# Kernel tuning notes

Measured on AMD Instinct MI355X. Metric: run time of the kernel, lower is better.

## Reference

```python
import jax, jax.numpy as jnp
import numpy as np

TAKE = 64
HID = 64


def setup_inputs() -> dict:
    key = jax.random.key(0)
    ks = jax.random.split(key, 12)
    B, N, C = 32, 1000, 1601
    s = 1.0 / np.sqrt(C)
    s2 = 1.0 / np.sqrt(HID)
    return {
        "class_logits": jax.random.normal(ks[0], (B, N, C), dtype=jnp.float32),
        "proposals": jax.random.uniform(ks[1], (B, N, 4), dtype=jnp.float32),
        # subject projection (Linear stored as [in, out] so y = x @ W + b)
        "Ws1": jax.random.uniform(ks[2], (C, HID), minval=-s, maxval=s),
        "bs1": jax.random.uniform(ks[3], (HID,), minval=-s, maxval=s),
        "Ws2": jax.random.uniform(ks[4], (HID, HID), minval=-s2, maxval=s2),
        "bs2": jax.random.uniform(ks[5], (HID,), minval=-s2, maxval=s2),
        # object projection
        "Wo1": jax.random.uniform(ks[6], (C, HID), minval=-s, maxval=s),
        "bo1": jax.random.uniform(ks[7], (HID,), minval=-s, maxval=s),
        "Wo2": jax.random.uniform(ks[8], (HID, HID), minval=-s2, maxval=s2),
        "bo2": jax.random.uniform(ks[9], (HID,), minval=-s2, maxval=s2),
    }


def _mlp(x, W1, b1, W2, b2):
    # Linear -> ReLU -> Linear
    return jnp.maximum(x @ W1 + b1, 0.0) @ W2 + b2


def reference(class_logits, proposals, Ws1, bs1, Ws2, bs2, Wo1, bo1, Wo2, bo2):
    B, N, _ = class_logits.shape
    subj = _mlp(class_logits, Ws1, bs1, Ws2, bs2)  # [B, N, 64]
    obj = _mlp(class_logits, Wo1, bo1, Wo2, bo2)   # [B, N, 64]
    # relatedness[b, i, j] = sigmoid(<subj_i, obj_j>)
    scores = jax.nn.sigmoid(jnp.einsum("bnd,bmd->bnm", subj, obj))  # [B, N, N]
    flat = scores.reshape(B, N * N)
    top_scores, top_idx = jax.lax.top_k(flat, TAKE)  # descending, same as sort[:take]
    # flat index k = subject*N + object (row-major), matching the torch meshgrid
    pairs = jnp.stack([top_idx // N, top_idx % N], axis=-1)  # [B, 64, 2] (subj, obj)
    return pairs, top_scores
```

## Files before the change

kernel.cpp:

```cpp
#include <hip/hip_runtime.h>
#include <cstdint>

#define NB 32
#define NN 1000
#define NC 1601
#define HID 64
#define ROWS (NB*NN)
#define CAPB 15360
#define SROWS 15
#define NBIN 4096
#define KCH 32
#define RB 64
#define TPB 256
#define XSTR 68
#define WSTR 132
#define SSTR 132

__device__ __forceinline__ uint32_t f2key(float f){
  uint32_t u = __float_as_uint(f);
  return (u & 0x80000000u) ? ~u : (u | 0x80000000u);
}
__device__ __forceinline__ float key2f(uint32_t k){
  uint32_t u = (k & 0x80000000u) ? (k & 0x7fffffffu) : ~k;
  return __uint_as_float(u);
}

__global__ __launch_bounds__(TPB, 2) void mlp_kernel(
    const float* __restrict__ x,
    const float* __restrict__ Ws1, const float* __restrict__ bs1,
    const float* __restrict__ Ws2, const float* __restrict__ bs2,
    const float* __restrict__ Wo1, const float* __restrict__ bo1,
    const float* __restrict__ Wo2, const float* __restrict__ bo2,
    float* __restrict__ subj, float* __restrict__ obj)
{
  __shared__ float smem[2*KCH*XSTR + 2*KCH*WSTR];
  __shared__ float xtail[RB];
  const int tid = threadIdx.x;
  const int tx  = tid & 15;
  const int ty  = tid >> 4;
  const int row0 = blockIdx.x * RB;

  float* xbuf = smem;
  float* wbuf = smem + 2*KCH*XSTR;

  float accS[4][4], accO[4][4];
  #pragma unroll
  for (int r=0;r<4;r++)
    #pragma unroll
    for (int c=0;c<4;c++){ accS[r][c]=0.f; accO[r][c]=0.f; }

  float  xstg[8];
  float4 wstg[4];
  #pragma unroll
  for (int it=0; it<8; it++){
    int u = tid + it*TPB;
    xstg[it] = x[(size_t)(row0 + (u>>5))*NC + (u&31)];
  }
  #pragma unroll
  for (int it=0; it<4; it++){
    int u = tid + it*TPB;
    int k = u>>5, c4 = u&31;
    const float* src = (c4 < 16) ? (Ws1 + (size_t)k*HID + c4*4)
                                 : (Wo1 + (size_t)k*HID + (c4-16)*4);
    wstg[it] = *(const float4*)src;
  }

  const int NCHUNK = 50;
  for (int c = 0; c < NCHUNK; c++){
    float* xT = xbuf + (c & 1)*(KCH*XSTR);
    float* wC = wbuf + (c & 1)*(KCH*WSTR);
    #pragma unroll
    for (int it=0; it<8; it++){
      int u = tid + it*TPB;
      xT[(u&31)*XSTR + (u>>5)] = xstg[it];
    }
    #pragma unroll
    for (int it=0; it<4; it++){
      int u = tid + it*TPB;
      *(float4*)&wC[(u>>5)*WSTR + (u&31)*4] = wstg[it];
    }
    __syncthreads();
    if (c+1 < NCHUNK){
      const int k0n = (c+1)*KCH;
      #pragma unroll
      for (int it=0; it<8; it++){
        int u = tid + it*TPB;
        xstg[it] = x[(size_t)(row0 + (u>>5))*NC + k0n + (u&31)];
      }
      #pragma unroll
      for (int it=0; it<4; it++){
        int u = tid + it*TPB;
        int k = u>>5, c4 = u&31;
        const float* src = (c4 < 16) ? (Ws1 + (size_t)(k0n+k)*HID + c4*4)
                                     : (Wo1 + (size_t)(k0n+k)*HID + (c4-16)*4);
        wstg[it] = *(const float4*)src;
      }
    }
    #pragma unroll 4
    for (int k=0; k<KCH; k++){
      float4 a  = *(const float4*)&xT[k*XSTR + ty*4];
      float4 bS = *(const float4*)&wC[k*WSTR + tx*4];
      float4 bO = *(const float4*)&wC[k*WSTR + 64 + tx*4];
      float av[4] = {a.x,a.y,a.z,a.w};
      float bs_[4] = {bS.x,bS.y,bS.z,bS.w};
      float bo_[4] = {bO.x,bO.y,bO.z,bO.w};
      #pragma unroll
      for (int r=0;r<4;r++)
        #pragma unroll
        for (int c2=0;c2<4;c2++){
          accS[r][c2] = fmaf(av[r], bs_[c2], accS[r][c2]);
          accO[r][c2] = fmaf(av[r], bo_[c2], accO[r][c2]);
        }
    }
  }

  if (tid < RB) xtail[tid] = x[(size_t)(row0 + tid)*NC + 1600];
  __syncthreads();
  {
    float4 a  = *(const float4*)&xtail[ty*4];
    float4 bS = *(const float4*)(Ws1 + (size_t)1600*HID + tx*4);
    float4 bO = *(const float4*)(Wo1 + (size_t)1600*HID + tx*4);
    float av[4] = {a.x,a.y,a.z,a.w};
    float bs_[4] = {bS.x,bS.y,bS.z,bS.w};
    float bo_[4] = {bO.x,bO.y,bO.z,bO.w};
    #pragma unroll
    for (int r=0;r<4;r++)
      #pragma unroll
      for (int c2=0;c2<4;c2++){
        accS[r][c2] = fmaf(av[r], bs_[c2], accS[r][c2]);
        accO[r][c2] = fmaf(av[r], bo_[c2], accO[r][c2]);
      }
  }

  float* hTS = smem;
  float* hTO = smem + 64*XSTR;
  __syncthreads();
  #pragma unroll
  for (int jj=0; jj<4; jj++){
    float bS = bs1[tx*4 + jj];
    float bO = bo1[tx*4 + jj];
    float4 hv;
    hv.x = fmaxf(accS[0][jj]+bS, 0.f); hv.y = fmaxf(accS[1][jj]+bS, 0.f);
    hv.z = fmaxf(accS[2][jj]+bS, 0.f); hv.w = fmaxf(accS[3][jj]+bS, 0.f);
    *(float4*)&hTS[(tx*4+jj)*XSTR + ty*4] = hv;
    hv.x = fmaxf(accO[0][jj]+bO, 0.f); hv.y = fmaxf(accO[1][jj]+bO, 0.f);
    hv.z = fmaxf(accO[2][jj]+bO, 0.f); hv.w = fmaxf(accO[3][jj]+bO, 0.f);
    *(float4*)&hTO[(tx*4+jj)*XSTR + ty*4] = hv;
  }
  __syncthreads();

  float accYS[4][4], accYO[4][4];
  #pragma unroll
  for (int c2=0;c2<4;c2++){
    float bvS = bs2[tx*4 + c2];
    float bvO = bo2[tx*4 + c2];
    #pragma unroll
    for (int r=0;r<4;r++){ accYS[r][c2] = bvS; accYO[r][c2] = bvO; }
  }
  #pragma unroll 4
  for (int d=0; d<64; d++){
    float4 aS = *(const float4*)&hTS[d*XSTR + ty*4];
    float4 aO = *(const float4*)&hTO[d*XSTR + ty*4];
    float4 wS = *(const float4*)(Ws2 + (size_t)d*HID + tx*4);
    float4 wO = *(const float4*)(Wo2 + (size_t)d*HID + tx*4);
    float aSv[4] = {aS.x,aS.y,aS.z,aS.w};
    float aOv[4] = {aO.x,aO.y,aO.z,aO.w};
    float wSv[4] = {wS.x,wS.y,wS.z,wS.w};
    float wOv[4] = {wO.x,wO.y,wO.z,wO.w};
    #pragma unroll
    for (int r=0;r<4;r++)
      #pragma unroll
      for (int c2=0;c2<4;c2++){
        accYS[r][c2] = fmaf(aSv[r], wSv[c2], accYS[r][c2]);
        accYO[r][c2] = fmaf(aOv[r], wOv[c2], accYO[r][c2]);
      }
  }
  #pragma unroll
  for (int r=0;r<4;r++){
    *(float4*)&subj[(size_t)(row0 + ty*4 + r)*HID + tx*4] =
      make_float4(accYS[r][0], accYS[r][1], accYS[r][2], accYS[r][3]);
    *(float4*)&obj[(size_t)(row0 + ty*4 + r)*HID + tx*4] =
      make_float4(accYO[r][0], accYO[r][1], accYO[r][2], accYO[r][3]);
  }
}

__global__ __launch_bounds__(1024, 4) void sample_thresh(
    const float* __restrict__ subj, const float* __restrict__ obj,
    uint32_t* __restrict__ L)
{
  __shared__ float sRows[SROWS*HID];
  __shared__ uint32_t keys[SROWS*NN];
  __shared__ uint32_t hist[256];
  __shared__ uint32_t sb[2];
  const int b = blockIdx.x, tid = threadIdx.x;

  const float4* sp = (const float4*)(subj + (size_t)b*NN*HID);
  if (tid < SROWS*16) ((float4*)sRows)[tid] = sp[tid];
  __syncthreads();

  for (int j = tid; j < NN; j += 1024){
    const float4* op4 = (const float4*)(obj + ((size_t)b*NN + j)*HID);
    float4 o[16];
    #pragma unroll
    for (int q=0;q<16;q++) o[q] = op4[q];
    #pragma unroll 1
    for (int i=0;i<SROWS;i++){
      const float4* s4 = (const float4*)(sRows + i*HID);
      float acc = 0.f;
      #pragma unroll
      for (int q=0;q<16;q++){
        float4 s = s4[q];
        acc = fmaf(s.x, o[q].x, acc); acc = fmaf(s.y, o[q].y, acc);
        acc = fmaf(s.z, o[q].z, acc); acc = fmaf(s.w, o[q].w, acc);
      }
      keys[i*NN + j] = f2key(acc);
    }
  }
  __syncthreads();

  uint32_t prefix = 0; int remaining = 64;
  for (int round = 0; round < 2; round++){
    const int shift = 24 - round*8;
    if (tid < 256) hist[tid] = 0;
    __syncthreads();
    for (int idx = tid; idx < SROWS*NN; idx += 1024){
      uint32_t k = keys[idx];
      bool match = (round == 0) || ((k >> 24) == (prefix >> 24));
      if (match) atomicAdd(&hist[(k >> shift) & 255u], 1u);
    }
    __syncthreads();
    if (tid == 0){
      uint32_t cum = 0; int bin = 255;
      for (;; bin--){ cum += hist[bin]; if (cum >= (uint32_t)remaining || bin == 0) break; }
      sb[0] = (uint32_t)bin;
      sb[1] = (uint32_t)(remaining - (int)(cum - hist[bin]));
    }
    __syncthreads();
    prefix |= sb[0] << shift;
    remaining = (int)sb[1];
    __syncthreads();
  }
  if (tid == 0) L[b] = prefix;
}

__device__ __forceinline__ void score_tile_acc(
    const float* __restrict__ subj, const float* __restrict__ obj,
    int b, int ti, int tj, int tid,
    float* __restrict__ sT, float* __restrict__ oT, float (&acc)[8][8])
{
  const int tx = tid & 15, ty = tid >> 4;
  #pragma unroll
  for (int a=0;a<8;a++)
    #pragma unroll
    for (int c=0;c<8;c++) acc[a][c] = 0.f;

  #pragma unroll 1
  for (int half = 0; half < 2; half++){
    __syncthreads();
    {
      const float4* gp = (const float4*)subj;
      #pragma unroll
      for (int it=0; it<4; it++){
        int u = tid + it*256;
        int r = u >> 3, q = (u & 7) + half*8;
        int gr = b*NN + ti + r; gr = gr < ROWS ? gr : (ROWS-1);
        float4 v = gp[(size_t)gr*16 + q];
        int kk = (u & 7)*4;
        sT[(kk+0)*SSTR + r] = v.x;
        sT[(kk+1)*SSTR + r] = v.y;
        sT[(kk+2)*SSTR + r] = v.z;
        sT[(kk+3)*SSTR + r] = v.w;
      }
      const float4* gp2 = (const float4*)obj;
      #pragma unroll
      for (int it=0; it<4; it++){
        int u = tid + it*256;
        int r = u >> 3, q = (u & 7) + half*8;
        int gr = b*NN + tj + r; gr = gr < ROWS ? gr : (ROWS-1);
        float4 v = gp2[(size_t)gr*16 + q];
        int kk = (u & 7)*4;
        oT[(kk+0)*SSTR + r] = v.x;
        oT[(kk+1)*SSTR + r] = v.y;
        oT[(kk+2)*SSTR + r] = v.z;
        oT[(kk+3)*SSTR + r] = v.w;
      }
    }
    __syncthreads();
    #pragma unroll 2
    for (int k=0; k<32; k++){
      float4 s0 = *(const float4*)&sT[k*SSTR + ty*8];
      float4 s1 = *(const float4*)&sT[k*SSTR + ty*8 + 4];
      float4 o0 = *(const float4*)&oT[k*SSTR + tx*8];
      float4 o1 = *(const float4*)&oT[k*SSTR + tx*8 + 4];
      float s[8] = {s0.x,s0.y,s0.z,s0.w,s1.x,s1.y,s1.z,s1.w};
      float o[8] = {o0.x,o0.y,o0.z,o0.w,o1.x,o1.y,o1.z,o1.w};
      #pragma unroll
      for (int a=0;a<8;a++)
        #pragma unroll
        for (int c=0;c<8;c++)
          acc[a][c] = fmaf(s[a], o[c], acc[a][c]);
    }
  }
}

__global__ __launch_bounds__(256, 3) void score_pass1(
    const float* __restrict__ subj, const float* __restrict__ obj,
    const uint32_t* __restrict__ L, uint32_t* __restrict__ cnt,
    uint2* __restrict__ cand, uint32_t* __restrict__ ghist)
{
  __shared__ float sT[32*SSTR];
  __shared__ float oT[32*SSTR];
  __shared__ uint32_t hist[NBIN];
  __shared__ uint32_t lcnt, gbase;
  const int blk = blockIdx.x;
  const int b   = blk >> 6;
  const int t   = blk & 63;
  const int ti  = (t >> 3) << 7;
  const int tj  = (t & 7)  << 7;
  const int tid = threadIdx.x;
  const int tx = tid & 15, ty = tid >> 4;

  for (int i = tid; i < NBIN; i += 256) hist[i] = 0;
  if (tid == 0) lcnt = 0;

  float acc[8][8];
  score_tile_acc(subj, obj, b, ti, tj, tid, sT, oT, acc);

  const uint32_t Lb = L[b];
  int myCnt = 0;
  #pragma unroll
  for (int a=0;a<8;a++){
    int gi = ti + ty*8 + a;
    #pragma unroll
    for (int c=0;c<8;c++){
      int gj = tj + tx*8 + c;
      if (gi < NN && gj < NN){
        uint32_t key = f2key(acc[a][c]);
        if (key >= Lb){ myCnt++; atomicAdd(&hist[key >> 20], 1u); }
      }
    }
  }
  uint32_t lbase = atomicAdd(&lcnt, (uint32_t)myCnt);
  __syncthreads();
  if (tid == 0) gbase = atomicAdd(&cnt[b], lcnt);
  __syncthreads();
  uint32_t pos = gbase + lbase;
  #pragma unroll
  for (int a=0;a<8;a++){
    int gi = ti + ty*8 + a;
    #pragma unroll
    for (int c=0;c<8;c++){
      int gj = tj + tx*8 + c;
      if (gi < NN && gj < NN){
        uint32_t key = f2key(acc[a][c]);
        if (key >= Lb){
          if (pos < CAPB) cand[(size_t)b*CAPB + pos] = make_uint2(key, (uint32_t)(gi*NN + gj));
          pos++;
        }
      }
    }
  }
  __syncthreads();
  for (int i = tid; i < NBIN; i += 256){
    uint32_t v = hist[i];
    if (v) atomicAdd(&ghist[(size_t)b*NBIN + i], v);
  }
}

__global__ __launch_bounds__(256, 1) void pick_thresh(
    const uint32_t* __restrict__ ghist, const uint32_t* __restrict__ cnt,
    uint32_t* __restrict__ T, uint32_t* __restrict__ flag)
{
  __shared__ uint32_t S[256];
  const int b = blockIdx.x, tid = threadIdx.x;
  const uint32_t* h = ghist + (size_t)b*NBIN;
  uint32_t loc[16];
  uint32_t s = 0;
  #pragma unroll
  for (int i=0;i<16;i++){ loc[i] = h[tid*16 + i]; s += loc[i]; }
  S[tid] = s;
  __syncthreads();
  for (int off = 1; off < 256; off <<= 1){
    uint32_t v = (tid + off < 256) ? S[tid + off] : 0u;
    __syncthreads();
    S[tid] += v;
    __syncthreads();
  }
  uint32_t above = (tid < 255) ? S[tid + 1] : 0u;
  if (above < 64u && S[tid] >= 64u){
    uint32_t suf = above; int best = 0;
    for (int i=15;i>=0;i--){ suf += loc[i]; if (suf >= 64u){ best = i; break; } }
    T[b] = (uint32_t)(tid*16 + best) << 20;
  }
  if (tid == 0) flag[b] = (cnt[b] > (uint32_t)CAPB) ? 1u : 0u;
}

__global__ __launch_bounds__(256, 3) void score_repair(
    const float* __restrict__ subj, const float* __restrict__ obj,
    const uint32_t* __restrict__ T, const uint32_t* __restrict__ flag,
    uint32_t* __restrict__ cnt2, uint2* __restrict__ cand)
{
  const int blk = blockIdx.x;
  const int b   = blk >> 6;
  if (flag[b] == 0u) return;

  __shared__ float sT[32*SSTR];
  __shared__ float oT[32*SSTR];
  __shared__ uint32_t lcnt, gbase;
  const int t   = blk & 63;
  const int ti  = (t >> 3) << 7;
  const int tj  = (t & 7)  << 7;
  const int tid = threadIdx.x;
  const int tx = tid & 15, ty = tid >> 4;

  if (tid == 0) lcnt = 0;

  float acc[8][8];
  score_tile_acc(subj, obj, b, ti, tj, tid, sT, oT, acc);

  const uint32_t Tb = T[b];
  int myCnt = 0;
  #pragma unroll
  for (int a=0;a<8;a++){
    int gi = ti + ty*8 + a;
    #pragma unroll
    for (int c=0;c<8;c++){
      int gj = tj + tx*8 + c;
      if (gi < NN && gj < NN && f2key(acc[a][c]) >= Tb) myCnt++;
    }
  }
  uint32_t lbase = atomicAdd(&lcnt, (uint32_t)myCnt);
  __syncthreads();
  if (tid == 0) gbase = atomicAdd(&cnt2[b], lcnt);
  __syncthreads();
  uint32_t pos = gbase + lbase;
  #pragma unroll
  for (int a=0;a<8;a++){
    int gi = ti + ty*8 + a;
    #pragma unroll
    for (int c=0;c<8;c++){
      int gj = tj + tx*8 + c;
      if (gi < NN && gj < NN){
        uint32_t key = f2key(acc[a][c]);
        if (key >= Tb){
          if (pos < CAPB) cand[(size_t)b*CAPB + pos] = make_uint2(key, (uint32_t)(gi*NN + gj));
          pos++;
        }
      }
    }
  }
}

__global__ __launch_bounds__(1024, 4) void final_select(
    const uint32_t* __restrict__ cnt, const uint32_t* __restrict__ cnt2,
    const uint32_t* __restrict__ flag, const uint2* __restrict__ cand,
    float* __restrict__ out)
{
  __shared__ uint32_t keys[CAPB];
  __shared__ uint32_t hist[256];
  __shared__ uint32_t sb[2];
  __shared__ uint2 win[192];
  __shared__ uint32_t wn;
  const int b = blockIdx.x, tid = threadIdx.x;
  uint32_t n0 = flag[b] ? cnt2[b] : cnt[b];
  const int n = (n0 < (uint32_t)CAPB) ? (int)n0 : CAPB;

  for (int i = tid; i < n; i += 1024) keys[i] = cand[(size_t)b*CAPB + i].x;
  if (tid == 0) wn = 0;
  __syncthreads();

  uint32_t prefix = 0; int remaining = 64;
  for (int round = 0; round < 4; round++){
    const int shift = 24 - round*8;
    if (tid < 256) hist[tid] = 0;
    __syncthreads();
    for (int i = tid; i < n; i += 1024){
      uint32_t k = keys[i];
      bool match = (round == 0) || ((k >> (shift+8)) == (prefix >> (shift+8)));
      if (match) atomicAdd(&hist[(k >> shift) & 255u], 1u);
    }
    __syncthreads();
    if (tid == 0){
      uint32_t cum = 0; int bin = 255;
      for (;; bin--){ cum += hist[bin]; if (cum >= (uint32_t)remaining || bin == 0) break; }
      sb[0] = (uint32_t)bin;
      sb[1] = (uint32_t)(remaining - (int)(cum - hist[bin]));
    }
    __syncthreads();
    prefix |= sb[0] << shift;
    remaining = (int)sb[1];
    __syncthreads();
  }
  const uint32_t Tk = prefix;

  for (int i = tid; i < n; i += 1024){
    if (keys[i] >= Tk){
      uint32_t p = atomicAdd(&wn, 1u);
      if (p < 192u) win[p] = make_uint2(keys[i], cand[(size_t)b*CAPB + i].y);
    }
  }
  __syncthreads();
  const int m = (wn < 192u) ? (int)wn : 192;

  if (tid < m){
    const uint64_t me = ((uint64_t)win[tid].x << 32) | (uint64_t)(uint32_t)(~win[tid].y);
    int rank = 0;
    for (int s = 0; s < m; s++){
      uint64_t oth = ((uint64_t)win[s].x << 32) | (uint64_t)(uint32_t)(~win[s].y);
      rank += (oth > me) ? 1 : 0;
    }
    if (rank < 64){
      const uint32_t f = win[tid].y;
      const float d  = key2f(win[tid].x);
      const float sc = 1.0f / (1.0f + expf(-d));
      out[((size_t)b*64 + rank)*2 + 0] = (float)(f / NN);
      out[((size_t)b*64 + rank)*2 + 1] = (float)(f % NN);
      out[(size_t)NB*64*2 + (size_t)b*64 + rank] = sc;
    }
  }
}

extern "C" void kernel_launch(void* const* d_in, const int* in_sizes, int n_in,
                              void* d_out, int out_size, void* d_ws, size_t ws_size,
                              hipStream_t stream) {
  const float* x   = (const float*)d_in[0];
  const float* Ws1 = (const float*)d_in[2];
  const float* bs1 = (const float*)d_in[3];
  const float* Ws2 = (const float*)d_in[4];
  const float* bs2 = (const float*)d_in[5];
  const float* Wo1 = (const float*)d_in[6];
  const float* bo1 = (const float*)d_in[7];
  const float* Wo2 = (const float*)d_in[8];
  const float* bo2 = (const float*)d_in[9];
  float* out = (float*)d_out;

  char* ws = (char*)d_ws;
  float*    subj = (float*)ws;
  float*    objp = (float*)(ws + 8192000);
  uint32_t* L    = (uint32_t*)(ws + 16384000);
  uint32_t* cnt  = (uint32_t*)(ws + 16384128);
  uint32_t* cnt2 = (uint32_t*)(ws + 16384256);
  uint32_t* ghist= (uint32_t*)(ws + 16384384);
  uint32_t* T    = (uint32_t*)(ws + 16908672);
  uint32_t* flag = (uint32_t*)(ws + 16908800);
  uint2*    cand = (uint2*)   (ws + 16908928);

  hipMemsetAsync(cnt, 0, 128 + 128 + 524288, stream);

  mlp_kernel<<<ROWS/RB, TPB, 0, stream>>>(x, Ws1, bs1, Ws2, bs2,
                                          Wo1, bo1, Wo2, bo2, subj, objp);
  sample_thresh<<<NB, 1024, 0, stream>>>(subj, objp, L);
  score_pass1<<<NB*64, 256, 0, stream>>>(subj, objp, L, cnt, cand, ghist);
  pick_thresh<<<NB, 256, 0, stream>>>(ghist, cnt, T, flag);
  score_repair<<<NB*64, 256, 0, stream>>>(subj, objp, T, flag, cnt2, cand);
  final_select<<<NB, 1024, 0, stream>>>(cnt, cnt2, flag, cand, out);
}
```

Measured before the change: 630.4 us.

## Fold workspace zeroing into sample_thresh and batch LDS loads in MLP inner loop

Removes the separate hipMemsetAsync launch by having each sample_thresh block zero its own histogram slice and counters before they are used by score_pass1. Separately, the MLP GEMM inner loop is restructured to load four k-steps of x and weight tiles from shared memory up front before the FMAs, to expose more load-level parallelism. This raises register pressure in the MLP kernel and relies on stream ordering for the zeroing to precede later kernels.

```diff
diff --git a/kernel.cpp b/kernel.cpp
--- a/kernel.cpp
+++ b/kernel.cpp
@@ -96,21 +96,36 @@
         wstg[it] = *(const float4*)src;
       }
     }
-    #pragma unroll 4
-    for (int k=0; k<KCH; k++){
-      float4 a  = *(const float4*)&xT[k*XSTR + ty*4];
-      float4 bS = *(const float4*)&wC[k*WSTR + tx*4];
-      float4 bO = *(const float4*)&wC[k*WSTR + 64 + tx*4];
-      float av[4] = {a.x,a.y,a.z,a.w};
-      float bs_[4] = {bS.x,bS.y,bS.z,bS.w};
-      float bo_[4] = {bO.x,bO.y,bO.z,bO.w};
-      #pragma unroll
-      for (int r=0;r<4;r++)
+    #pragma unroll 2
+    for (int k=0; k<KCH; k+=4){
+      float4 A0 = *(const float4*)&xT[(k+0)*XSTR + ty*4];
+      float4 A1 = *(const float4*)&xT[(k+1)*XSTR + ty*4];
+      float4 A2 = *(const float4*)&xT[(k+2)*XSTR + ty*4];
+      float4 A3 = *(const float4*)&xT[(k+3)*XSTR + ty*4];
+      float4 S0 = *(const float4*)&wC[(k+0)*WSTR + tx*4];
+      float4 S1 = *(const float4*)&wC[(k+1)*WSTR + tx*4];
+      float4 S2 = *(const float4*)&wC[(k+2)*WSTR + tx*4];
+      float4 S3 = *(const float4*)&wC[(k+3)*WSTR + tx*4];
+      float4 O0 = *(const float4*)&wC[(k+0)*WSTR + 64 + tx*4];
+      float4 O1 = *(const float4*)&wC[(k+1)*WSTR + 64 + tx*4];
+      float4 O2 = *(const float4*)&wC[(k+2)*WSTR + 64 + tx*4];
+      float4 O3 = *(const float4*)&wC[(k+3)*WSTR + 64 + tx*4];
+      #pragma unroll
+      for (int kk=0; kk<4; kk++){
+        float4 A = kk==0?A0 : kk==1?A1 : kk==2?A2 : A3;
+        float4 S = kk==0?S0 : kk==1?S1 : kk==2?S2 : S3;
+        float4 O = kk==0?O0 : kk==1?O1 : kk==2?O2 : O3;
+        float av[4] = {A.x,A.y,A.z,A.w};
+        float bs_[4] = {S.x,S.y,S.z,S.w};
+        float bo_[4] = {O.x,O.y,O.z,O.w};
         #pragma unroll
-        for (int c2=0;c2<4;c2++){
-          accS[r][c2] = fmaf(av[r], bs_[c2], accS[r][c2]);
-          accO[r][c2] = fmaf(av[r], bo_[c2], accO[r][c2]);
-        }
+        for (int r=0;r<4;r++)
+          #pragma unroll
+          for (int c2=0;c2<4;c2++){
+            accS[r][c2] = fmaf(av[r], bs_[c2], accS[r][c2]);
+            accO[r][c2] = fmaf(av[r], bo_[c2], accO[r][c2]);
+          }
+      }
     }
   }
 
@@ -186,13 +201,18 @@
 
 __global__ __launch_bounds__(1024, 4) void sample_thresh(
     const float* __restrict__ subj, const float* __restrict__ obj,
-    uint32_t* __restrict__ L)
+    uint32_t* __restrict__ L, uint32_t* __restrict__ cnt,
+    uint32_t* __restrict__ cnt2, uint32_t* __restrict__ ghist)
 {
   __shared__ float sRows[SROWS*HID];
   __shared__ uint32_t keys[SROWS*NN];
   __shared__ uint32_t hist[256];
   __shared__ uint32_t sb[2];
   const int b = blockIdx.x, tid = threadIdx.x;
+
+  uint32_t* gh = ghist + (size_t)b*NBIN;
+  for (int i = tid; i < NBIN; i += 1024) gh[i] = 0u;
+  if (tid == 0){ cnt[b] = 0u; cnt2[b] = 0u; }
 
   const float4* sp = (const float4*)(subj + (size_t)b*NN*HID);
   if (tid < SROWS*16) ((float4*)sRows)[tid] = sp[tid];
@@ -545,11 +565,9 @@
   uint32_t* flag = (uint32_t*)(ws + 16908800);
   uint2*    cand = (uint2*)   (ws + 16908928);
 
-  hipMemsetAsync(cnt, 0, 128 + 128 + 524288, stream);
-
   mlp_kernel<<<ROWS/RB, TPB, 0, stream>>>(x, Ws1, bs1, Ws2, bs2,
                                           Wo1, bo1, Wo2, bo2, subj, objp);
-  sample_thresh<<<NB, 1024, 0, stream>>>(subj, objp, L);
+  sample_thresh<<<NB, 1024, 0, stream>>>(subj, objp, L, cnt, cnt2, ghist);
   score_pass1<<<NB*64, 256, 0, stream>>>(subj, objp, L, cnt, cand, ghist);
   pick_thresh<<<NB, 256, 0, stream>>>(ghist, cnt, T, flag);
   score_repair<<<NB*64, 256, 0, stream>>>(subj, objp, T, flag, cnt2, cand);
```

New measurement: 617.6 us. 2.0% less time.
